# Performance work log

Hardware: AMD Instinct MI355X
Metric: run time of the kernel (lower is better)

Reference implementation:

```python
import jax, jax.numpy as jnp
import numpy as np

N = 50000      # nodes
E = 400000     # edges (avg degree 8)
G = 256        # graphs in batch
H = 256        # hidden_dim
DEPTH = 6
A, C, X, EF = 16, 8, 3, 16  # a_t, c_t, x_t, e_t feature dims (node_feats=27)


def setup_inputs() -> dict:
    key = jax.random.key(0)
    ks = jax.random.split(key, 16)
    s = lambda i, shape, sc=1.0: jax.random.normal(ks[i], shape, jnp.float32) * sc
    return {
        "a_t": s(0, (N, A)),
        "c_t": s(1, (N, C)),
        "x_t": s(2, (N, X)),
        "e_t": s(3, (E, EF)),
        "src": jax.random.randint(ks[4], (E,), 0, N),
        "dst": jax.random.randint(ks[5], (E,), 0, N),
        "graph_id": jnp.sort(jax.random.randint(ks[6], (N,), 0, G)),
        "W_in": s(7, (A + C + X, H), 0.1), "b_in": jnp.zeros((H,), jnp.float32),
        "W_e": s(8, (EF, H), 0.1), "b_e": jnp.zeros((H,), jnp.float32),
        "Wc1": s(9, (DEPTH, H, H), 0.05), "bc1": jnp.zeros((DEPTH, H), jnp.float32),
        "g1": jnp.ones((DEPTH, H), jnp.float32), "be1": jnp.zeros((DEPTH, H), jnp.float32),
        "Wc2": s(10, (DEPTH, H, H), 0.05), "bc2": jnp.zeros((DEPTH, H), jnp.float32),
        "g2": jnp.ones((DEPTH, H), jnp.float32), "be2": jnp.zeros((DEPTH, H), jnp.float32),
        "W_head": s(11, (H, 1), 0.1), "b_head": jnp.zeros((1,), jnp.float32),
    }


def _ln(x, g, b):
    mu = jnp.mean(x, -1, keepdims=True)
    v = jnp.mean((x - mu) ** 2, -1, keepdims=True)
    return (x - mu) * jax.lax.rsqrt(v + 1e-5) * g + b


def reference(a_t, c_t, x_t, e_t, src, dst, graph_id,
              W_in, b_in, W_e, b_e,
              Wc1, bc1, g1, be1, Wc2, bc2, g2, be2,
              W_head, b_head):
    n = a_t.shape[0]
    ones_e = jnp.ones((src.shape[0],), jnp.float32)
    deg_out = jax.ops.segment_sum(ones_e, src, num_segments=n)
    deg_in = jax.ops.segment_sum(ones_e, dst, num_segments=n)
    # DGL GraphConv norm='both': 0 for isolated nodes (pow(0,-0.5)=inf -> 0)
    norm_o = jnp.where(deg_out > 0, jax.lax.rsqrt(jnp.maximum(deg_out, 1.0)), 0.0)
    norm_i = jnp.where(deg_in > 0, jax.lax.rsqrt(jnp.maximum(deg_in, 1.0)), 0.0)

    def gconv(x, W, b):
        h = (x * norm_o[:, None]) @ W            # [N,H] transform + src norm
        m = jax.ops.segment_sum(h[src], dst, num_segments=n)  # SpMM gather/scatter
        return m * norm_i[:, None] + b

    h = gconv(jnp.concatenate([a_t, c_t, x_t], -1), W_in, b_in)
    e = e_t @ W_e + b_e                          # edge_linear
    # copy_e + mean over in-edges
    e_mean = jax.ops.segment_sum(e, dst, num_segments=n) / jnp.maximum(deg_in, 1.0)[:, None]
    h = h + e_mean

    def body(hc, p):
        W1, b1, ga, ba, W2, b2, gb, bb = p
        t = jax.nn.silu(_ln(gconv(hc, W1, b1), ga, ba))
        t = jax.nn.silu(_ln(gconv(t, W2, b2), gb, bb))
        return t + hc, None  # skip is Identity (in_dim == out_dim)

    h, _ = jax.lax.scan(body, h, (Wc1, bc1, g1, be1, Wc2, bc2, g2, be2))

    cnt = jax.ops.segment_sum(jnp.ones((n,), jnp.float32), graph_id, num_segments=G)
    pooled = jax.ops.segment_sum(h, graph_id, num_segments=G) / jnp.maximum(cnt, 1.0)[:, None]
    # property='dipole' -> Softplus, tau=1.0
    return jax.nn.softplus((pooled @ W_head + b_head) / 1.0)
```

## Files before the change

### kernel.cpp

```cpp
#include <hip/hip_runtime.h>
#include <hip/hip_bf16.h>

#define N_NODES 50000
#define N_EDGES 400000
#define N_GRAPH 256
#define HID 256
#define DEPTH 6

typedef float f32x4 __attribute__((ext_vector_type(4)));
typedef int   i32x4 __attribute__((ext_vector_type(4)));

__device__ __forceinline__ float bf2f(unsigned short u) {
  unsigned v = ((unsigned)u) << 16;
  return __builtin_bit_cast(float, v);
}
__device__ __forceinline__ unsigned short f2bf(float f) {
  unsigned u = __builtin_bit_cast(unsigned, f);
  u += 0x7fffu + ((u >> 16) & 1u);
  return (unsigned short)(u >> 16);
}

__device__ __forceinline__ float block_sum256(float v, float* lds) {
#pragma unroll
  for (int off = 32; off > 0; off >>= 1) v += __shfl_down(v, off, 64);
  int w = threadIdx.x >> 6;
  if ((threadIdx.x & 63) == 0) lds[w] = v;
  __syncthreads();
  float r = lds[0] + lds[1] + lds[2] + lds[3];
  __syncthreads();
  return r;
}

__global__ __launch_bounds__(256) void k_deg(const int* __restrict__ src, const int* __restrict__ dst,
                                             int* deg_out, int* deg_in) {
  int e = blockIdx.x * 256 + threadIdx.x;
  if (e < N_EDGES) { atomicAdd(&deg_out[src[e]], 1); atomicAdd(&deg_in[dst[e]], 1); }
}

__global__ __launch_bounds__(256) void k_norm(const int* deg_out, const int* deg_in,
                                              float* norm_o, float* norm_i) {
  int i = blockIdx.x * 256 + threadIdx.x;
  if (i < N_NODES) {
    int dO = deg_out[i], dI = deg_in[i];
    norm_o[i] = dO > 0 ? rsqrtf((float)dO) : 0.f;
    norm_i[i] = dI > 0 ? rsqrtf((float)dI) : 0.f;
  }
}

__global__ __launch_bounds__(256) void k_scan1(const int* deg_in, int* partial) {
  int i = blockIdx.x * 256 + threadIdx.x;
  int v = (i < N_NODES) ? deg_in[i] : 0;
#pragma unroll
  for (int off = 32; off > 0; off >>= 1) v += __shfl_down(v, off, 64);
  __shared__ int l[4];
  if ((threadIdx.x & 63) == 0) l[threadIdx.x >> 6] = v;
  __syncthreads();
  if (threadIdx.x == 0) partial[blockIdx.x] = l[0] + l[1] + l[2] + l[3];
}

__global__ __launch_bounds__(256) void k_scan2(const int* partial, int* chunk_off, int* row_start, int nb) {
  __shared__ int ss[256];
  int t = threadIdx.x;
  int v = (t < nb) ? partial[t] : 0;
  ss[t] = v; __syncthreads();
#pragma unroll
  for (int off = 1; off < 256; off <<= 1) {
    int x = ss[t];
    int y = (t >= off) ? ss[t - off] : 0;
    __syncthreads();
    ss[t] = x + y;
    __syncthreads();
  }
  if (t < nb) chunk_off[t] = ss[t] - v;
  if (t == 0) row_start[N_NODES] = N_EDGES;
}

__global__ __launch_bounds__(256) void k_scan3(const int* deg_in, const int* chunk_off, int* row_start) {
  __shared__ int ss[256];
  int t = threadIdx.x;
  int i = blockIdx.x * 256 + t;
  int v = (i < N_NODES) ? deg_in[i] : 0;
  ss[t] = v; __syncthreads();
#pragma unroll
  for (int off = 1; off < 256; off <<= 1) {
    int x = ss[t];
    int y = (t >= off) ? ss[t - off] : 0;
    __syncthreads();
    ss[t] = x + y;
    __syncthreads();
  }
  if (i < N_NODES) row_start[i] = chunk_off[blockIdx.x] + ss[t] - v;
}

__global__ __launch_bounds__(256) void k_fill(const int* src, const int* dst, const int* row_start,
                                              int* cursor, int* csr_src, int* csr_eid) {
  int e = blockIdx.x * 256 + threadIdx.x;
  if (e < N_EDGES) {
    int d = dst[e];
    int p = atomicAdd(&cursor[d], 1);
    int pos = row_start[d] + p;
    csr_src[pos] = src[e];
    csr_eid[pos] = e;
  }
}

__global__ __launch_bounds__(256) void k_wt(const float* __restrict__ Wc1, const float* __restrict__ Wc2,
                                            unsigned short* __restrict__ Wt) {
  __shared__ float tile[32][33];
  int li = blockIdx.z;
  const float* W = ((li & 1) ? Wc2 : Wc1) + (size_t)(li >> 1) * HID * HID;
  int k0 = blockIdx.x * 32, n0 = blockIdx.y * 32;
  int tx = threadIdx.x & 31, ty = threadIdx.x >> 5;
#pragma unroll
  for (int r = ty; r < 32; r += 8) tile[r][tx] = W[(size_t)(k0 + r) * HID + n0 + tx];
  __syncthreads();
  unsigned short* outp = Wt + (size_t)li * HID * HID;
#pragma unroll
  for (int r = ty; r < 32; r += 8) outp[(size_t)(n0 + r) * HID + k0 + tx] = f2bf(tile[tx][r]);
}

__global__ __launch_bounds__(256) void k_z(const float* __restrict__ a, const float* __restrict__ c,
                                           const float* __restrict__ x, const float* __restrict__ norm_o,
                                           float* __restrict__ z) {
  int t = blockIdx.x * 256 + threadIdx.x;
  int n = t >> 5, lane = t & 31;
  if (n >= N_NODES) return;
  float v = 0.f;
  if (lane < 16) v = a[(size_t)n * 16 + lane];
  else if (lane < 24) v = c[(size_t)n * 8 + (lane - 16)];
  else if (lane < 27) v = x[(size_t)n * 3 + (lane - 24)];
  z[(size_t)n * 32 + lane] = v * norm_o[n];
}

__global__ __launch_bounds__(256) void k_in(const float* __restrict__ z, const float* __restrict__ e_t,
                                            const int* __restrict__ csr_src, const int* __restrict__ csr_eid,
                                            const int* __restrict__ rs, const float* __restrict__ norm_o,
                                            const float* __restrict__ norm_i, const float* __restrict__ W_in,
                                            const float* __restrict__ b_in, const float* __restrict__ W_e,
                                            const float* __restrict__ b_e, float* __restrict__ hf,
                                            unsigned short* __restrict__ Af) {
  int w = threadIdx.x >> 6, lane = threadIdx.x & 63;
  int n = blockIdx.x * 4 + w;
  __shared__ float zs[4][48];
  int beg = rs[n], end = rs[n + 1];
  float acc = 0.f;
  for (int p = beg; p < end; ++p) {
    if (lane < 27) acc += z[(size_t)csr_src[p] * 32 + lane];
    else if (lane >= 32 && lane < 48) acc += e_t[(size_t)csr_eid[p] * 16 + (lane - 32)];
  }
  if (lane < 27) zs[w][lane] = acc;
  else if (lane >= 32 && lane < 48) zs[w][27 + lane - 32] = acc;
  __syncthreads();
  float degf = (float)(end - beg);
  float invd = 1.f / fmaxf(degf, 1.f);
  float niv = norm_i[n], nov = norm_o[n];
#pragma unroll
  for (int i = 0; i < 4; ++i) {
    int ch = lane + 64 * i;
    float da = 0.f, de = 0.f;
#pragma unroll
    for (int k = 0; k < 27; ++k) da += zs[w][k] * W_in[k * HID + ch];
#pragma unroll
    for (int k = 0; k < 16; ++k) de += zs[w][27 + k] * W_e[k * HID + ch];
    float val = da * niv + b_in[ch] + (de + degf * b_e[ch]) * invd;
    hf[(size_t)n * HID + ch] = val;
    Af[(size_t)n * HID + ch] = f2bf(val * nov);
  }
}

template <int RES>
__global__ __launch_bounds__(256) void k_layer(const unsigned short* __restrict__ Af,
                                               const int* __restrict__ csr_src, const int* __restrict__ rs,
                                               const unsigned short* __restrict__ Bt,
                                               const float* __restrict__ norm_i,
                                               const float* __restrict__ norm_o,
                                               const float* __restrict__ b, const float* __restrict__ g,
                                               const float* __restrict__ be, float* __restrict__ hf,
                                               unsigned short* __restrict__ AfN) {
  const int LDA = HID + 8;
  __shared__ unsigned short As[16 * LDA];
  __shared__ float red1[4][16], red2[4][16];
  int wave = threadIdx.x >> 6, lane = threadIdx.x & 63;
  int l15 = lane & 15, quad = lane >> 4;
  int n0 = blockIdx.x * 16;
  int off = lane * 4;
  for (int i = 0; i < 4; ++i) {
    int r = wave * 4 + i;
    int beg = rs[n0 + r], end = rs[n0 + r + 1];
    float a0 = 0.f, a1 = 0.f, a2 = 0.f, a3 = 0.f;
    int p = beg;
    for (; p + 4 <= end; p += 4) {
      int s0 = csr_src[p], s1 = csr_src[p + 1], s2 = csr_src[p + 2], s3 = csr_src[p + 3];
      ushort4 r0 = *(const ushort4*)(Af + (size_t)s0 * HID + off);
      ushort4 r1 = *(const ushort4*)(Af + (size_t)s1 * HID + off);
      ushort4 r2 = *(const ushort4*)(Af + (size_t)s2 * HID + off);
      ushort4 r3 = *(const ushort4*)(Af + (size_t)s3 * HID + off);
      a0 += bf2f(r0.x) + bf2f(r1.x) + bf2f(r2.x) + bf2f(r3.x);
      a1 += bf2f(r0.y) + bf2f(r1.y) + bf2f(r2.y) + bf2f(r3.y);
      a2 += bf2f(r0.z) + bf2f(r1.z) + bf2f(r2.z) + bf2f(r3.z);
      a3 += bf2f(r0.w) + bf2f(r1.w) + bf2f(r2.w) + bf2f(r3.w);
    }
    for (; p < end; ++p) {
      int s0 = csr_src[p];
      ushort4 r0 = *(const ushort4*)(Af + (size_t)s0 * HID + off);
      a0 += bf2f(r0.x); a1 += bf2f(r0.y); a2 += bf2f(r0.z); a3 += bf2f(r0.w);
    }
    ushort4 o;
    o.x = f2bf(a0); o.y = f2bf(a1); o.z = f2bf(a2); o.w = f2bf(a3);
    *(ushort4*)(&As[(size_t)r * LDA + off]) = o;
  }
  __syncthreads();
  const unsigned short* asp = &As[(size_t)l15 * LDA + quad * 8];
  const unsigned short* bp = Bt + (size_t)(wave * 64 + l15) * HID + quad * 8;
  f32x4 acc[4] = {};
  asm volatile("s_nop 7\n\ts_nop 7" : "+v"(acc[0]), "+v"(acc[1]), "+v"(acc[2]), "+v"(acc[3]));
#pragma unroll
  for (int k0 = 0; k0 < HID; k0 += 32) {
    i32x4 af = *(const i32x4*)(asp + k0);
#pragma unroll
    for (int t = 0; t < 4; ++t) {
      i32x4 bt = *(const i32x4*)(bp + (size_t)t * 16 * HID + k0);
      asm volatile("v_mfma_f32_16x16x32_bf16 %0, %1, %2, %0" : "+v"(acc[t]) : "v"(af), "v"(bt));
    }
  }
  asm volatile("s_nop 7\n\ts_nop 7\n\ts_nop 7"
               : "+v"(acc[0]), "+v"(acc[1]), "+v"(acc[2]), "+v"(acc[3]));
  float ni[4];
#pragma unroll
  for (int j = 0; j < 4; ++j) ni[j] = norm_i[n0 + quad * 4 + j];
#pragma unroll
  for (int t = 0; t < 4; ++t) {
    int ct = wave * 64 + t * 16 + l15;
    float bv = b[ct];
#pragma unroll
    for (int j = 0; j < 4; ++j) acc[t][j] = acc[t][j] * ni[j] + bv;
  }
  float s1[4] = {0.f, 0.f, 0.f, 0.f}, s2[4] = {0.f, 0.f, 0.f, 0.f};
#pragma unroll
  for (int t = 0; t < 4; ++t)
#pragma unroll
    for (int j = 0; j < 4; ++j) { s1[j] += acc[t][j]; s2[j] += acc[t][j] * acc[t][j]; }
#pragma unroll
  for (int m = 1; m < 16; m <<= 1) {
#pragma unroll
    for (int j = 0; j < 4; ++j) {
      s1[j] += __shfl_xor(s1[j], m, 16);
      s2[j] += __shfl_xor(s2[j], m, 16);
    }
  }
  if (l15 == 0) {
#pragma unroll
    for (int j = 0; j < 4; ++j) {
      red1[wave][quad * 4 + j] = s1[j];
      red2[wave][quad * 4 + j] = s2[j];
    }
  }
  __syncthreads();
  float mu[4], inv[4];
#pragma unroll
  for (int j = 0; j < 4; ++j) {
    int r = quad * 4 + j;
    float t1 = red1[0][r] + red1[1][r] + red1[2][r] + red1[3][r];
    float t2 = red2[0][r] + red2[1][r] + red2[2][r] + red2[3][r];
    mu[j] = t1 * (1.f / HID);
    float var = t2 * (1.f / HID) - mu[j] * mu[j];
    inv[j] = rsqrtf(var + 1e-5f);
  }
#pragma unroll
  for (int j = 0; j < 4; ++j) {
    int r = n0 + quad * 4 + j;
    float nov = norm_o[r];
    float* hrow = hf + (size_t)r * HID;
    unsigned short* an = AfN + (size_t)r * HID;
#pragma unroll
    for (int t = 0; t < 4; ++t) {
      int ct = wave * 64 + t * 16 + l15;
      float o = (acc[t][j] - mu[j]) * inv[j] * g[ct] + be[ct];
      float sl = o * (1.f / (1.f + __expf(-o)));
      float outv = sl;
      if (RES) {
        outv = sl + hrow[ct];
        hrow[ct] = outv;
      }
      an[ct] = f2bf(outv * nov);
    }
  }
}

__global__ __launch_bounds__(256) void k_poolhead(const float* __restrict__ hf, const int* __restrict__ gid,
                                                  const float* __restrict__ Wh, const float* __restrict__ bh,
                                                  float* __restrict__ out) {
  int gg = blockIdx.x, ch = threadIdx.x;
  int lo = 0, hi = N_NODES;
  while (lo < hi) { int mid = (lo + hi) >> 1; if (gid[mid] < gg) lo = mid + 1; else hi = mid; }
  int beg = lo;
  hi = N_NODES;
  while (lo < hi) { int mid = (lo + hi) >> 1; if (gid[mid] < gg + 1) lo = mid + 1; else hi = mid; }
  int end = lo;
  float s = 0.f;
  int n = beg;
  for (; n + 4 <= end; n += 4) {
    s += hf[(size_t)n * HID + ch] + hf[(size_t)(n + 1) * HID + ch] +
         hf[(size_t)(n + 2) * HID + ch] + hf[(size_t)(n + 3) * HID + ch];
  }
  for (; n < end; ++n) s += hf[(size_t)n * HID + ch];
  float v = s * Wh[ch];
  __shared__ float l[4];
  float tot = block_sum256(v, l);
  if (ch == 0) {
    float c = fmaxf((float)(end - beg), 1.f);
    float xx = tot / c + bh[0];
    out[gg] = fmaxf(xx, 0.f) + log1pf(expf(-fabsf(xx)));
  }
}

extern "C" void kernel_launch(void* const* d_in, const int* in_sizes, int n_in,
                              void* d_out, int out_size, void* d_ws, size_t ws_size,
                              hipStream_t stream) {
  const float* a_t = (const float*)d_in[0];
  const float* c_t = (const float*)d_in[1];
  const float* x_t = (const float*)d_in[2];
  const float* e_t = (const float*)d_in[3];
  const int* src = (const int*)d_in[4];
  const int* dst = (const int*)d_in[5];
  const int* gid = (const int*)d_in[6];
  const float* W_in = (const float*)d_in[7];
  const float* b_in = (const float*)d_in[8];
  const float* W_e  = (const float*)d_in[9];
  const float* b_e  = (const float*)d_in[10];
  const float* Wc1  = (const float*)d_in[11];
  const float* bc1  = (const float*)d_in[12];
  const float* g1   = (const float*)d_in[13];
  const float* be1  = (const float*)d_in[14];
  const float* Wc2  = (const float*)d_in[15];
  const float* bc2  = (const float*)d_in[16];
  const float* g2   = (const float*)d_in[17];
  const float* be2  = (const float*)d_in[18];
  const float* W_head = (const float*)d_in[19];
  const float* b_head = (const float*)d_in[20];
  float* out = (float*)d_out;

  char* base = (char*)d_ws;
  size_t off = 0;
  auto carve = [&](size_t bytes) -> void* {
    void* p = base + off;
    off += (bytes + 255) & ~(size_t)255;
    return p;
  };
  int*   deg_out = (int*)carve((size_t)N_NODES * 4);
  int*   deg_in  = (int*)carve((size_t)N_NODES * 4);
  int*   cursor  = (int*)carve((size_t)N_NODES * 4);
  size_t zbytes = off;
  float* norm_o  = (float*)carve((size_t)N_NODES * 4);
  float* norm_i  = (float*)carve((size_t)N_NODES * 4);
  int*   row_start = (int*)carve((size_t)(N_NODES + 1) * 4);
  int*   partial   = (int*)carve(256 * 4);
  int*   chunk_off = (int*)carve(256 * 4);
  int*   csr_src   = (int*)carve((size_t)N_EDGES * 4);
  int*   csr_eid   = (int*)carve((size_t)N_EDGES * 4);
  unsigned short* Wt = (unsigned short*)carve((size_t)2 * DEPTH * HID * HID * 2);
  float* zpack = (float*)carve((size_t)N_NODES * 32 * 4);
  float* hf = (float*)carve((size_t)N_NODES * HID * 4);
  unsigned short* Af0 = (unsigned short*)carve((size_t)N_NODES * HID * 2);
  unsigned short* Af1 = (unsigned short*)carve((size_t)N_NODES * HID * 2);
  (void)ws_size; (void)in_sizes; (void)n_in; (void)out_size;

  hipMemsetAsync(d_ws, 0, zbytes, stream);

  int ebl = (N_EDGES + 255) / 256;
  int nbl = (N_NODES + 255) / 256;
  k_deg<<<ebl, 256, 0, stream>>>(src, dst, deg_out, deg_in);
  k_norm<<<nbl, 256, 0, stream>>>(deg_out, deg_in, norm_o, norm_i);
  k_scan1<<<nbl, 256, 0, stream>>>(deg_in, partial);
  k_scan2<<<1, 256, 0, stream>>>(partial, chunk_off, row_start, nbl);
  k_scan3<<<nbl, 256, 0, stream>>>(deg_in, chunk_off, row_start);
  k_fill<<<ebl, 256, 0, stream>>>(src, dst, row_start, cursor, csr_src, csr_eid);
  k_wt<<<dim3(8, 8, 2 * DEPTH), 256, 0, stream>>>(Wc1, Wc2, Wt);
  k_z<<<(N_NODES * 32 + 255) / 256, 256, 0, stream>>>(a_t, c_t, x_t, norm_o, zpack);
  k_in<<<N_NODES / 4, 256, 0, stream>>>(zpack, e_t, csr_src, csr_eid, row_start,
                                        norm_o, norm_i, W_in, b_in, W_e, b_e, hf, Af0);
  int gbl = N_NODES / 16;
  for (int d = 0; d < DEPTH; ++d) {
    k_layer<0><<<gbl, 256, 0, stream>>>(Af0, csr_src, row_start, Wt + (size_t)(2 * d) * HID * HID,
                                        norm_i, norm_o, bc1 + d * HID, g1 + d * HID, be1 + d * HID, hf, Af1);
    k_layer<1><<<gbl, 256, 0, stream>>>(Af1, csr_src, row_start, Wt + (size_t)(2 * d + 1) * HID * HID,
                                        norm_i, norm_o, bc2 + d * HID, g2 + d * HID, be2 + d * HID, hf, Af0);
  }
  k_poolhead<<<N_GRAPH, 256, 0, stream>>>(hf, gid, W_head, b_head, out);
}
```

Measured before the change: 1.493 ms.

## Use 512-thread layer blocks, bf16 residual, atomic edge-feature sums

Several changes land at once. The layer kernel now runs 8 waves per block, each gathering two rows in a single merged 8-wide loop and owning 32 output columns of the MFMA GEMM. The residual buffer hf is stored in bf16 instead of fp32, halving its traffic in every residual layer and in pooling. Edge-feature sums are precomputed with a separate atomic scatter kernel, which removes csr_eid, and the input gather is split across two half-waves. These aim to raise latency hiding in the gather and cut memory traffic, at the cost of bf16 rounding accumulating in the residual stream and nondeterministic atomic float sums.

```diff
diff --git a/kernel.cpp b/kernel.cpp
--- a/kernel.cpp
+++ b/kernel.cpp
@@ -93,15 +93,20 @@
 }
 
 __global__ __launch_bounds__(256) void k_fill(const int* src, const int* dst, const int* row_start,
-                                              int* cursor, int* csr_src, int* csr_eid) {
+                                              int* cursor, int* csr_src) {
   int e = blockIdx.x * 256 + threadIdx.x;
   if (e < N_EDGES) {
     int d = dst[e];
     int p = atomicAdd(&cursor[d], 1);
-    int pos = row_start[d] + p;
-    csr_src[pos] = src[e];
-    csr_eid[pos] = e;
-  }
+    csr_src[row_start[d] + p] = src[e];
+  }
+}
+
+__global__ __launch_bounds__(256) void k_esum(const float* __restrict__ e_t, const int* __restrict__ dst,
+                                              float* esum) {
+  int t = blockIdx.x * 256 + threadIdx.x;
+  int e = t >> 4, ch = t & 15;
+  if (e < N_EDGES) atomicAdd(&esum[(size_t)dst[e] * 16 + ch], e_t[(size_t)e * 16 + ch]);
 }
 
 __global__ __launch_bounds__(256) void k_wt(const float* __restrict__ Wc1, const float* __restrict__ Wc2,
@@ -132,112 +137,124 @@
   z[(size_t)n * 32 + lane] = v * norm_o[n];
 }
 
-__global__ __launch_bounds__(256) void k_in(const float* __restrict__ z, const float* __restrict__ e_t,
-                                            const int* __restrict__ csr_src, const int* __restrict__ csr_eid,
-                                            const int* __restrict__ rs, const float* __restrict__ norm_o,
-                                            const float* __restrict__ norm_i, const float* __restrict__ W_in,
-                                            const float* __restrict__ b_in, const float* __restrict__ W_e,
-                                            const float* __restrict__ b_e, float* __restrict__ hf,
-                                            unsigned short* __restrict__ Af) {
+__global__ __launch_bounds__(256) void k_in(const float* __restrict__ z, const float* __restrict__ esum,
+                                            const int* __restrict__ csr_src, const int* __restrict__ rs,
+                                            const float* __restrict__ norm_o, const float* __restrict__ norm_i,
+                                            const float* __restrict__ W_in, const float* __restrict__ b_in,
+                                            const float* __restrict__ W_e, const float* __restrict__ b_e,
+                                            unsigned short* __restrict__ hf, unsigned short* __restrict__ Af) {
   int w = threadIdx.x >> 6, lane = threadIdx.x & 63;
   int n = blockIdx.x * 4 + w;
-  __shared__ float zs[4][48];
+  int half = lane >> 5, ch = lane & 31;
+  __shared__ float zs[4][32];
+  __shared__ float es[4][16];
+  if (lane >= 32 && lane < 48) es[w][lane - 32] = esum[(size_t)n * 16 + (lane - 32)];
   int beg = rs[n], end = rs[n + 1];
   float acc = 0.f;
-  for (int p = beg; p < end; ++p) {
-    if (lane < 27) acc += z[(size_t)csr_src[p] * 32 + lane];
-    else if (lane >= 32 && lane < 48) acc += e_t[(size_t)csr_eid[p] * 16 + (lane - 32)];
-  }
-  if (lane < 27) zs[w][lane] = acc;
-  else if (lane >= 32 && lane < 48) zs[w][27 + lane - 32] = acc;
+  const float* zb = z + ch;
+  int p = beg + half;
+  for (; p + 6 < end; p += 8) {
+    int s0 = csr_src[p], s1 = csr_src[p + 2], s2 = csr_src[p + 4], s3 = csr_src[p + 6];
+    float v0 = zb[(size_t)s0 * 32], v1 = zb[(size_t)s1 * 32];
+    float v2 = zb[(size_t)s2 * 32], v3 = zb[(size_t)s3 * 32];
+    acc += (v0 + v1) + (v2 + v3);
+  }
+  for (; p < end; p += 2) acc += zb[(size_t)csr_src[p] * 32];
+  acc += __shfl_xor(acc, 32, 64);
+  if (lane < 32) zs[w][ch] = acc;
   __syncthreads();
   float degf = (float)(end - beg);
   float invd = 1.f / fmaxf(degf, 1.f);
   float niv = norm_i[n], nov = norm_o[n];
 #pragma unroll
   for (int i = 0; i < 4; ++i) {
-    int ch = lane + 64 * i;
+    int cc = lane + 64 * i;
     float da = 0.f, de = 0.f;
 #pragma unroll
-    for (int k = 0; k < 27; ++k) da += zs[w][k] * W_in[k * HID + ch];
-#pragma unroll
-    for (int k = 0; k < 16; ++k) de += zs[w][27 + k] * W_e[k * HID + ch];
-    float val = da * niv + b_in[ch] + (de + degf * b_e[ch]) * invd;
-    hf[(size_t)n * HID + ch] = val;
-    Af[(size_t)n * HID + ch] = f2bf(val * nov);
+    for (int k = 0; k < 27; ++k) da += zs[w][k] * W_in[k * HID + cc];
+#pragma unroll
+    for (int k = 0; k < 16; ++k) de += es[w][k] * W_e[k * HID + cc];
+    float val = da * niv + b_in[cc] + (de + degf * b_e[cc]) * invd;
+    hf[(size_t)n * HID + cc] = f2bf(val);
+    Af[(size_t)n * HID + cc] = f2bf(val * nov);
   }
 }
 
 template <int RES>
-__global__ __launch_bounds__(256) void k_layer(const unsigned short* __restrict__ Af,
+__global__ __launch_bounds__(512) void k_layer(const unsigned short* __restrict__ Af,
                                                const int* __restrict__ csr_src, const int* __restrict__ rs,
                                                const unsigned short* __restrict__ Bt,
                                                const float* __restrict__ norm_i,
                                                const float* __restrict__ norm_o,
                                                const float* __restrict__ b, const float* __restrict__ g,
-                                               const float* __restrict__ be, float* __restrict__ hf,
+                                               const float* __restrict__ be,
+                                               unsigned short* __restrict__ hf,
                                                unsigned short* __restrict__ AfN) {
   const int LDA = HID + 8;
   __shared__ unsigned short As[16 * LDA];
-  __shared__ float red1[4][16], red2[4][16];
+  __shared__ float red1[8][16], red2[8][16];
   int wave = threadIdx.x >> 6, lane = threadIdx.x & 63;
   int l15 = lane & 15, quad = lane >> 4;
   int n0 = blockIdx.x * 16;
   int off = lane * 4;
-  for (int i = 0; i < 4; ++i) {
-    int r = wave * 4 + i;
-    int beg = rs[n0 + r], end = rs[n0 + r + 1];
-    float a0 = 0.f, a1 = 0.f, a2 = 0.f, a3 = 0.f;
-    int p = beg;
-    for (; p + 4 <= end; p += 4) {
-      int s0 = csr_src[p], s1 = csr_src[p + 1], s2 = csr_src[p + 2], s3 = csr_src[p + 3];
-      ushort4 r0 = *(const ushort4*)(Af + (size_t)s0 * HID + off);
-      ushort4 r1 = *(const ushort4*)(Af + (size_t)s1 * HID + off);
-      ushort4 r2 = *(const ushort4*)(Af + (size_t)s2 * HID + off);
-      ushort4 r3 = *(const ushort4*)(Af + (size_t)s3 * HID + off);
-      a0 += bf2f(r0.x) + bf2f(r1.x) + bf2f(r2.x) + bf2f(r3.x);
-      a1 += bf2f(r0.y) + bf2f(r1.y) + bf2f(r2.y) + bf2f(r3.y);
-      a2 += bf2f(r0.z) + bf2f(r1.z) + bf2f(r2.z) + bf2f(r3.z);
-      a3 += bf2f(r0.w) + bf2f(r1.w) + bf2f(r2.w) + bf2f(r3.w);
+  int r0 = wave * 2;
+  int beg = rs[n0 + r0], mid = rs[n0 + r0 + 1], end = rs[n0 + r0 + 2];
+  float lo0 = 0.f, lo1 = 0.f, lo2 = 0.f, lo3 = 0.f;
+  float hi0 = 0.f, hi1 = 0.f, hi2 = 0.f, hi3 = 0.f;
+  int p = beg;
+  for (; p + 8 <= end; p += 8) {
+    int s[8];
+#pragma unroll
+    for (int q = 0; q < 8; ++q) s[q] = csr_src[p + q];
+    ushort4 rr[8];
+#pragma unroll
+    for (int q = 0; q < 8; ++q) rr[q] = *(const ushort4*)(Af + (size_t)s[q] * HID + off);
+#pragma unroll
+    for (int q = 0; q < 8; ++q) {
+      float v0 = bf2f(rr[q].x), v1 = bf2f(rr[q].y), v2 = bf2f(rr[q].z), v3 = bf2f(rr[q].w);
+      if (p + q >= mid) { hi0 += v0; hi1 += v1; hi2 += v2; hi3 += v3; }
+      else             { lo0 += v0; lo1 += v1; lo2 += v2; lo3 += v3; }
     }
-    for (; p < end; ++p) {
-      int s0 = csr_src[p];
-      ushort4 r0 = *(const ushort4*)(Af + (size_t)s0 * HID + off);
-      a0 += bf2f(r0.x); a1 += bf2f(r0.y); a2 += bf2f(r0.z); a3 += bf2f(r0.w);
-    }
-    ushort4 o;
-    o.x = f2bf(a0); o.y = f2bf(a1); o.z = f2bf(a2); o.w = f2bf(a3);
-    *(ushort4*)(&As[(size_t)r * LDA + off]) = o;
-  }
+  }
+  for (; p < end; ++p) {
+    ushort4 r = *(const ushort4*)(Af + (size_t)csr_src[p] * HID + off);
+    float v0 = bf2f(r.x), v1 = bf2f(r.y), v2 = bf2f(r.z), v3 = bf2f(r.w);
+    if (p >= mid) { hi0 += v0; hi1 += v1; hi2 += v2; hi3 += v3; }
+    else          { lo0 += v0; lo1 += v1; lo2 += v2; lo3 += v3; }
+  }
+  ushort4 o;
+  o.x = f2bf(lo0); o.y = f2bf(lo1); o.z = f2bf(lo2); o.w = f2bf(lo3);
+  *(ushort4*)(&As[(size_t)r0 * LDA + off]) = o;
+  o.x = f2bf(hi0); o.y = f2bf(hi1); o.z = f2bf(hi2); o.w = f2bf(hi3);
+  *(ushort4*)(&As[(size_t)(r0 + 1) * LDA + off]) = o;
   __syncthreads();
   const unsigned short* asp = &As[(size_t)l15 * LDA + quad * 8];
-  const unsigned short* bp = Bt + (size_t)(wave * 64 + l15) * HID + quad * 8;
-  f32x4 acc[4] = {};
-  asm volatile("s_nop 7\n\ts_nop 7" : "+v"(acc[0]), "+v"(acc[1]), "+v"(acc[2]), "+v"(acc[3]));
+  const unsigned short* bp = Bt + (size_t)(wave * 32 + l15) * HID + quad * 8;
+  f32x4 acc[2] = {};
+  asm volatile("s_nop 7\n\ts_nop 7" : "+v"(acc[0]), "+v"(acc[1]));
 #pragma unroll
   for (int k0 = 0; k0 < HID; k0 += 32) {
     i32x4 af = *(const i32x4*)(asp + k0);
 #pragma unroll
-    for (int t = 0; t < 4; ++t) {
+    for (int t = 0; t < 2; ++t) {
       i32x4 bt = *(const i32x4*)(bp + (size_t)t * 16 * HID + k0);
       asm volatile("v_mfma_f32_16x16x32_bf16 %0, %1, %2, %0" : "+v"(acc[t]) : "v"(af), "v"(bt));
     }
   }
-  asm volatile("s_nop 7\n\ts_nop 7\n\ts_nop 7"
-               : "+v"(acc[0]), "+v"(acc[1]), "+v"(acc[2]), "+v"(acc[3]));
+  asm volatile("s_nop 7\n\ts_nop 7\n\ts_nop 7" : "+v"(acc[0]), "+v"(acc[1]));
   float ni[4];
 #pragma unroll
   for (int j = 0; j < 4; ++j) ni[j] = norm_i[n0 + quad * 4 + j];
 #pragma unroll
-  for (int t = 0; t < 4; ++t) {
-    int ct = wave * 64 + t * 16 + l15;
+  for (int t = 0; t < 2; ++t) {
+    int ct = wave * 32 + t * 16 + l15;
     float bv = b[ct];
 #pragma unroll
     for (int j = 0; j < 4; ++j) acc[t][j] = acc[t][j] * ni[j] + bv;
   }
   float s1[4] = {0.f, 0.f, 0.f, 0.f}, s2[4] = {0.f, 0.f, 0.f, 0.f};
 #pragma unroll
-  for (int t = 0; t < 4; ++t)
+  for (int t = 0; t < 2; ++t)
 #pragma unroll
     for (int j = 0; j < 4; ++j) { s1[j] += acc[t][j]; s2[j] += acc[t][j] * acc[t][j]; }
 #pragma unroll
@@ -260,8 +277,9 @@
 #pragma unroll
   for (int j = 0; j < 4; ++j) {
     int r = quad * 4 + j;
-    float t1 = red1[0][r] + red1[1][r] + red1[2][r] + red1[3][r];
-    float t2 = red2[0][r] + red2[1][r] + red2[2][r] + red2[3][r];
+    float t1 = 0.f, t2 = 0.f;
+#pragma unroll
+    for (int ww = 0; ww < 8; ++ww) { t1 += red1[ww][r]; t2 += red2[ww][r]; }
     mu[j] = t1 * (1.f / HID);
     float var = t2 * (1.f / HID) - mu[j] * mu[j];
     inv[j] = rsqrtf(var + 1e-5f);
@@ -270,24 +288,25 @@
   for (int j = 0; j < 4; ++j) {
     int r = n0 + quad * 4 + j;
     float nov = norm_o[r];
-    float* hrow = hf + (size_t)r * HID;
+    unsigned short* hrow = hf + (size_t)r * HID;
     unsigned short* an = AfN + (size_t)r * HID;
 #pragma unroll
-    for (int t = 0; t < 4; ++t) {
-      int ct = wave * 64 + t * 16 + l15;
-      float o = (acc[t][j] - mu[j]) * inv[j] * g[ct] + be[ct];
-      float sl = o * (1.f / (1.f + __expf(-o)));
+    for (int t = 0; t < 2; ++t) {
+      int ct = wave * 32 + t * 16 + l15;
+      float oo = (acc[t][j] - mu[j]) * inv[j] * g[ct] + be[ct];
+      float sl = oo * (1.f / (1.f + __expf(-oo)));
       float outv = sl;
       if (RES) {
-        outv = sl + hrow[ct];
-        hrow[ct] = outv;
+        outv = sl + bf2f(hrow[ct]);
+        hrow[ct] = f2bf(outv);
       }
       an[ct] = f2bf(outv * nov);
     }
   }
 }
 
-__global__ __launch_bounds__(256) void k_poolhead(const float* __restrict__ hf, const int* __restrict__ gid,
+__global__ __launch_bounds__(256) void k_poolhead(const unsigned short* __restrict__ hf,
+                                                  const int* __restrict__ gid,
                                                   const float* __restrict__ Wh, const float* __restrict__ bh,
                                                   float* __restrict__ out) {
   int gg = blockIdx.x, ch = threadIdx.x;
@@ -300,10 +319,10 @@
   float s = 0.f;
   int n = beg;
   for (; n + 4 <= end; n += 4) {
-    s += hf[(size_t)n * HID + ch] + hf[(size_t)(n + 1) * HID + ch] +
-         hf[(size_t)(n + 2) * HID + ch] + hf[(size_t)(n + 3) * HID + ch];
-  }
-  for (; n < end; ++n) s += hf[(size_t)n * HID + ch];
+    s += bf2f(hf[(size_t)n * HID + ch]) + bf2f(hf[(size_t)(n + 1) * HID + ch]) +
+         bf2f(hf[(size_t)(n + 2) * HID + ch]) + bf2f(hf[(size_t)(n + 3) * HID + ch]);
+  }
+  for (; n < end; ++n) s += bf2f(hf[(size_t)n * HID + ch]);
   float v = s * Wh[ch];
   __shared__ float l[4];
   float tot = block_sum256(v, l);
@@ -350,6 +369,7 @@
   int*   deg_out = (int*)carve((size_t)N_NODES * 4);
   int*   deg_in  = (int*)carve((size_t)N_NODES * 4);
   int*   cursor  = (int*)carve((size_t)N_NODES * 4);
+  float* esum    = (float*)carve((size_t)N_NODES * 16 * 4);
   size_t zbytes = off;
   float* norm_o  = (float*)carve((size_t)N_NODES * 4);
   float* norm_i  = (float*)carve((size_t)N_NODES * 4);
@@ -357,10 +377,9 @@
   int*   partial   = (int*)carve(256 * 4);
   int*   chunk_off = (int*)carve(256 * 4);
   int*   csr_src   = (int*)carve((size_t)N_EDGES * 4);
-  int*   csr_eid   = (int*)carve((size_t)N_EDGES * 4);
   unsigned short* Wt = (unsigned short*)carve((size_t)2 * DEPTH * HID * HID * 2);
   float* zpack = (float*)carve((size_t)N_NODES * 32 * 4);
-  float* hf = (float*)carve((size_t)N_NODES * HID * 4);
+  unsigned short* hf = (unsigned short*)carve((size_t)N_NODES * HID * 2);
   unsigned short* Af0 = (unsigned short*)carve((size_t)N_NODES * HID * 2);
   unsigned short* Af1 = (unsigned short*)carve((size_t)N_NODES * HID * 2);
   (void)ws_size; (void)in_sizes; (void)n_in; (void)out_size;
@@ -374,16 +393,17 @@
   k_scan1<<<nbl, 256, 0, stream>>>(deg_in, partial);
   k_scan2<<<1, 256, 0, stream>>>(partial, chunk_off, row_start, nbl);
   k_scan3<<<nbl, 256, 0, stream>>>(deg_in, chunk_off, row_start);
-  k_fill<<<ebl, 256, 0, stream>>>(src, dst, row_start, cursor, csr_src, csr_eid);
+  k_fill<<<ebl, 256, 0, stream>>>(src, dst, row_start, cursor, csr_src);
+  k_esum<<<(N_EDGES * 16 + 255) / 256, 256, 0, stream>>>(e_t, dst, esum);
   k_wt<<<dim3(8, 8, 2 * DEPTH), 256, 0, stream>>>(Wc1, Wc2, Wt);
   k_z<<<(N_NODES * 32 + 255) / 256, 256, 0, stream>>>(a_t, c_t, x_t, norm_o, zpack);
-  k_in<<<N_NODES / 4, 256, 0, stream>>>(zpack, e_t, csr_src, csr_eid, row_start,
+  k_in<<<N_NODES / 4, 256, 0, stream>>>(zpack, esum, csr_src, row_start,
                                         norm_o, norm_i, W_in, b_in, W_e, b_e, hf, Af0);
   int gbl = N_NODES / 16;
   for (int d = 0; d < DEPTH; ++d) {
-    k_layer<0><<<gbl, 256, 0, stream>>>(Af0, csr_src, row_start, Wt + (size_t)(2 * d) * HID * HID,
+    k_layer<0><<<gbl, 512, 0, stream>>>(Af0, csr_src, row_start, Wt + (size_t)(2 * d) * HID * HID,
                                         norm_i, norm_o, bc1 + d * HID, g1 + d * HID, be1 + d * HID, hf, Af1);
-    k_layer<1><<<gbl, 256, 0, stream>>>(Af1, csr_src, row_start, Wt + (size_t)(2 * d + 1) * HID * HID,
+    k_layer<1><<<gbl, 512, 0, stream>>>(Af1, csr_src, row_start, Wt + (size_t)(2 * d + 1) * HID * HID,
                                         norm_i, norm_o, bc2 + d * HID, g2 + d * HID, be2 + d * HID, hf, Af0);
   }
   k_poolhead<<<N_GRAPH, 256, 0, stream>>>(hf, gid, W_head, b_head, out);
```

New measurement: 1.443 ms. -3.4%, faster.
